# Kernel optimization log

Measured on AMD Instinct MI355X. Metric: run time of the kernel, lower is better.

Reference implementation:

```python
import jax, jax.numpy as jnp
import numpy as np

B, N, H, DQK, DV = 2, 2048, 16, 128, 128
E = H * DV
CHUNK = 64


def setup_inputs() -> dict:
    key = jax.random.key(0)
    ks = jax.random.split(key, 11)
    w = lambda k: jax.random.normal(k, (E, E), jnp.float32) * 0.02
    return {
        "x": jax.random.normal(ks[0], (B, N, E), jnp.float32),
        "prev_state": jnp.zeros((B, H, DQK, DV), jnp.float32),
        "Wq": w(ks[1]), "bq": jnp.zeros((E,), jnp.float32),
        "Wk": w(ks[2]), "bk": jnp.zeros((E,), jnp.float32),
        "Wv": w(ks[3]), "bv": jnp.zeros((E,), jnp.float32),
        "Wg": w(ks[4]), "bg": jnp.zeros((E,), jnp.float32),
        "Wo": w(ks[5]), "bo": jnp.zeros((E,), jnp.float32),
        "start_idx": 0,
    }


def _mul_i(t):
    # multiply interleaved complex pairs by i: (a, b) -> (-b, a)
    t2 = t.reshape(*t.shape[:-1], -1, 2)
    return jnp.stack((-t2[..., 1], t2[..., 0]), axis=-1).reshape(t.shape)


def reference(x, prev_state, Wq, bq, Wk, bk, Wv, bv, Wg, bg, Wo, bo, start_idx):
    b, n, e = x.shape
    h, dqk, dv, c = H, DQK, DV, CHUNK
    q = (x @ Wq.T + bq).reshape(b, n, h, dqk)
    k = (x @ Wk.T + bk).reshape(b, n, h, dqk)
    v = (x @ Wv.T + bv).reshape(b, n, h, dv)

    # xPos-style theta shift (rotary on interleaved pairs), applied along the sequence dim
    lin = jnp.linspace(0.0, 1.0, dqk // 2)
    thetas = jnp.repeat(1.0 / (10000.0 ** lin), 2).astype(x.dtype)  # (dqk,)
    idx = (start_idx + jnp.arange(n)).astype(x.dtype)
    ang = idx[:, None] * thetas[None, :]  # (n, dqk)
    sin = jnp.sin(ang)[None, :, None, :]
    cos = jnp.cos(ang)[None, :, None, :]
    q = q * cos + _mul_i(q) * sin
    k = k * cos + _mul_i(k) * sin
    k = k / jnp.sqrt(jnp.asarray(dqk, x.dtype))

    # per-head decays: 1 - 2^(-5 - h)
    gamma = 1.0 - jnp.exp2(-5.0 - jnp.arange(h, dtype=x.dtype))  # (h,)
    i = jnp.arange(c, dtype=x.dtype)
    mask = i[:, None] >= i[None, :]
    Dmat = jnp.where(mask, gamma[:, None, None] ** jnp.where(mask, i[:, None] - i[None, :], 0.0), 0.0)  # (h,c,c)
    cross_decay = gamma[:, None] ** (i[None, :] + 1.0)   # (h,c)
    kv_decay = gamma[:, None] ** (c - 1.0 - i[None, :])  # (h,c)
    chunk_decay = gamma ** c                              # (h,)

    nc = n // c
    qc = q.reshape(b, nc, c, h, dqk).transpose(1, 0, 3, 2, 4)  # (nc,b,h,c,dqk)
    kc = k.reshape(b, nc, c, h, dqk).transpose(1, 0, 3, 2, 4)
    vc = v.reshape(b, nc, c, h, dv).transpose(1, 0, 3, 2, 4)

    def step(S, qkv):
        qi, ki, vi = qkv  # (b,h,c,d)
        att = jnp.einsum('bhid,bhjd->bhij', qi, ki) * Dmat[None]
        o = jnp.einsum('bhij,bhje->bhie', att, vi)
        o = o + jnp.einsum('bhid,bhde->bhie', qi, S) * cross_decay[None, :, :, None]
        S_new = S * chunk_decay[None, :, None, None] + jnp.einsum('bhjd,bhje->bhde', ki * kv_decay[None, :, :, None], vi)
        return S_new, o

    state, outs = jax.lax.scan(step, prev_state, (qc, kc, vc))
    ret = outs.transpose(1, 0, 3, 2, 4).reshape(b, n, h, dv)

    # GroupNorm(num_groups=h, affine=False): normalize each head over dv
    mu = ret.mean(-1, keepdims=True)
    var = ((ret - mu) ** 2).mean(-1, keepdims=True)
    ret = ((ret - mu) / jnp.sqrt(var + 1e-6)).reshape(b, n, e)

    gate = jax.nn.silu(x @ Wg.T + bg)
    out = (ret * gate) @ Wo.T + bo
    return out, state
```

## Files before the change

kernel.cpp:

```cpp
#include <hip/hip_runtime.h>
#include <hip/hip_bf16.h>
#include <stdint.h>

#define B_   2
#define N_   2048
#define H_   16
#define DQK_ 128
#define DV_  128
#define E_   2048
#define CH_  64
#define NC_  32
#define M_   (B_*N_)
#define QKVG_LD 8192
#define ROT_C 0.21091607f
#define KS_   0.08838834764831843f

using bf16x8 = __attribute__((ext_vector_type(8))) __bf16;
using f32x4  = __attribute__((ext_vector_type(4))) float;
typedef __hip_bfloat16 bf16_t;

__device__ __forceinline__ void gload_lds16(const void* g, void* l) {
  __builtin_amdgcn_global_load_lds(
      (const __attribute__((address_space(1))) void*)(uintptr_t)g,
      (__attribute__((address_space(3))) void*)(uint32_t)(uintptr_t)l,
      16, 0, 0);
}

__device__ __forceinline__ float head_log2g(int h) {
  return (float)(log2(1.0 - exp2((double)(-5 - h))));
}

__device__ __forceinline__ float bfu2f(unsigned short u) {
  unsigned int t = (unsigned int)u << 16; float f;
  __builtin_memcpy(&f, &t, 4); return f;
}
__device__ __forceinline__ unsigned short f2bfu(float f) {
  bf16_t b = __float2bfloat16(f);
  unsigned short u; __builtin_memcpy(&u, &b, 2); return u;
}

__global__ __launch_bounds__(256)
void cvt_all_kernel(const float* __restrict__ x,
                    const float* __restrict__ Wq, const float* __restrict__ Wk,
                    const float* __restrict__ Wv, const float* __restrict__ Wg,
                    const float* __restrict__ Wo,
                    const float* __restrict__ bq, const float* __restrict__ bk,
                    const float* __restrict__ bv, const float* __restrict__ bg,
                    const int* __restrict__ startp,
                    bf16_t* __restrict__ xb, bf16_t* __restrict__ wcat,
                    bf16_t* __restrict__ wob, float* __restrict__ bcat,
                    float2* __restrict__ trig) {
  const int NX = 2097152, NW = 1048576;
  int g = blockIdx.x * 256 + threadIdx.x;
  const float* s; bf16_t* d; int si, di;
  if (g < NX) { s = x; si = g; d = xb; di = g; }
  else if (g < NX + 4*NW) {
    int t = g - NX; int r = t / NW; si = t - r*NW;
    s = (r==0) ? Wq : (r==1) ? Wk : (r==2) ? Wv : Wg; d = wcat; di = t;
  } else if (g < NX + 5*NW) {
    si = g - NX - 4*NW; s = Wo; d = wob; di = si;
  } else if (g < NX + 5*NW + 2048) {
    int j = g - (NX + 5*NW);
    int which = j >> 9, i = j & 511;
    const float* bs = (which==0) ? bq : (which==1) ? bk : (which==2) ? bv : bg;
    ((float4*)bcat)[which*512 + i] = ((const float4*)bs)[i];
    return;
  } else {
    int g2 = g - (NX + 5*NW + 2048);
    if (g2 < 131072) {
      int n = g2 >> 6, j = g2 & 63;
      float ang = (float)(startp[0] + n) * exp2f(-ROT_C * (float)j);
      float sn, cn; sincosf(ang, &sn, &cn);
      trig[g2] = make_float2(cn, sn);
    }
    return;
  }
  float4 v = ((const float4*)s)[si];
  ushort4 p;
  p.x = f2bfu(v.x); p.y = f2bfu(v.y); p.z = f2bfu(v.z); p.w = f2bfu(v.w);
  ((ushort4*)d)[di] = p;
}

template<bool OUT_BF16, int NSUB>
__global__ __launch_bounds__(512, 2)
void gemm8_kernel(const bf16_t* __restrict__ A, const bf16_t* __restrict__ Bw,
                  const float* __restrict__ bias, void* __restrict__ Cout,
                  int K, int ldc, int tilesM) {
  extern __shared__ char smem[];
  const int nwg = gridDim.x;
  const int bid = blockIdx.x;
  const int cpx = nwg >> 3;
  const int swz = (bid & 7) * cpx + (bid >> 3);
  const int tm = swz % tilesM, tn = swz / tilesM;
  const int rowT0 = tm * 256, colT0 = tn * (64 * NSUB);
  const int tid = threadIdx.x, wave = tid >> 6, lane = tid & 63;
  const int wr = wave >> 2, wc = wave & 3;
  const int l16 = lane & 15, lhi = lane >> 4;
  const int NKT = K >> 6;

  const int sw = ((tid & 7) * 16) ^ (((tid >> 3) & 7) << 4);
  const size_t aOff = (size_t)(rowT0 + (tid >> 3)) * K + (sw >> 1);
  const size_t bOff = (size_t)(colT0 + (tid >> 3)) * K + (sw >> 1);
  const uint32_t wl = wave * 1024;

  auto stage = [&](int h) {
    const int ktp = h >> 2, r = h & 3, buf = ktp & 1;
    const int k0 = ktp << 6;
    if (r < 2) {
      const uint32_t base = 65536u + buf * (8192u*NSUB) + r * (4096u*NSUB) + wl;
#pragma unroll
      for (int L = 0; L < NSUB/2; L++)
        gload_lds16(Bw + bOff + (size_t)(r * (NSUB*32) + L * 64) * K + k0,
                    smem + base + L * 8192);
    } else {
      const int half = r - 2;
      const uint32_t base = buf * 32768u + half * 16384u + wl;
#pragma unroll
      for (int L = 0; L < 2; L++)
        gload_lds16(A + aOff + (size_t)(half * 128 + L * 64) * K + k0,
                    smem + base + L * 8192);
    }
  };

  for (int h = 0; h < 6; h++) stage(h);
  if constexpr (NSUB == 4) asm volatile("s_waitcnt vmcnt(4)" ::: "memory");
  else                     asm volatile("s_waitcnt vmcnt(2)" ::: "memory");
  __builtin_amdgcn_s_barrier();
  asm volatile("" ::: "memory");
  __builtin_amdgcn_sched_barrier(0);

  f32x4 acc[8][NSUB] = {};
  bf16x8 bfr[NSUB][2], bnx[2][2];

#pragma unroll
  for (int n = 0; n < 2; n++) {
    const int r = wc * (16*NSUB) + n * 16 + l16;
#pragma unroll
    for (int ks = 0; ks < 2; ks++) {
      const int cb = ks * 64 + lhi * 16;
      bnx[n][ks] = *(const bf16x8*)(smem + 65536u + r * 128 + (cb ^ ((r & 7) << 4)));
    }
  }

  for (int kt = 0; kt < NKT; kt++) {
    const int cur = kt & 1;
    const uint32_t aB = cur * 32768u;
    const uint32_t bB = 65536u + cur * (8192u*NSUB);
#pragma unroll
    for (int p = 0; p < 4; p++) {
      if (p == 0) {
#pragma unroll
        for (int n = 0; n < 2; n++)
#pragma unroll
          for (int ks = 0; ks < 2; ks++) bfr[n][ks] = bnx[n][ks];
        if constexpr (NSUB == 4) {
#pragma unroll
          for (int n = 2; n < 4; n++) {
            const int r = wc * (16*NSUB) + n * 16 + l16;
#pragma unroll
            for (int ks = 0; ks < 2; ks++) {
              const int cb = ks * 64 + lhi * 16;
              bfr[n][ks] = *(const bf16x8*)(smem + bB + r * 128 + (cb ^ ((r & 7) << 4)));
            }
          }
        }
      }
      bf16x8 afr[2][2];
#pragma unroll
      for (int mm = 0; mm < 2; mm++) {
        const int r = wr * 128 + p * 32 + mm * 16 + l16;
#pragma unroll
        for (int ks = 0; ks < 2; ks++) {
          const int cb = ks * 64 + lhi * 16;
          afr[mm][ks] = *(const bf16x8*)(smem + aB + r * 128 + (cb ^ ((r & 7) << 4)));
        }
      }
      const int h = 4 * kt + p + 6;
      if (h < 4 * NKT) stage(h);
      __builtin_amdgcn_sched_barrier(0);
      __builtin_amdgcn_s_setprio(1);
#pragma unroll
      for (int mm = 0; mm < 2; mm++)
#pragma unroll
        for (int n = 0; n < NSUB; n++)
#pragma unroll
          for (int ks = 0; ks < 2; ks++)
            acc[2 * p + mm][n] = __builtin_amdgcn_mfma_f32_16x16x32_bf16(
                afr[mm][ks], bfr[n][ks], acc[2 * p + mm][n], 0, 0, 0);
      __builtin_amdgcn_s_setprio(0);
      if (p == 2) {
        if constexpr (NSUB == 4) asm volatile("s_waitcnt vmcnt(6)" ::: "memory");
        else                     asm volatile("s_waitcnt vmcnt(5)" ::: "memory");
      }
      if (p == 3) {
        if (kt < NKT - 2) {
          if constexpr (NSUB == 4) asm volatile("s_waitcnt vmcnt(4)" ::: "memory");
          else                     asm volatile("s_waitcnt vmcnt(2)" ::: "memory");
        } else if (kt == NKT - 2) {
          asm volatile("s_waitcnt vmcnt(0)" ::: "memory");
        }
        if (kt + 1 < NKT) {
          const uint32_t bN = 65536u + ((kt + 1) & 1) * (8192u*NSUB);
#pragma unroll
          for (int n = 0; n < 2; n++) {
            const int r = wc * (16*NSUB) + n * 16 + l16;
#pragma unroll
            for (int ks = 0; ks < 2; ks++) {
              const int cb = ks * 64 + lhi * 16;
              bnx[n][ks] = *(const bf16x8*)(smem + bN + r * 128 + (cb ^ ((r & 7) << 4)));
            }
          }
        }
      }
      __builtin_amdgcn_s_barrier();
      asm volatile("" ::: "memory");
      __builtin_amdgcn_sched_barrier(0);
    }
  }

#pragma unroll
  for (int m = 0; m < 8; m++) {
    const int rbase = rowT0 + wr * 128 + m * 16 + lhi * 4;
#pragma unroll
    for (int n = 0; n < NSUB; n++) {
      const int col = colT0 + wc * (16*NSUB) + n * 16 + l16;
      const float bv = bias[col];
#pragma unroll
      for (int j = 0; j < 4; j++) {
        float v = acc[m][n][j] + bv;
        if (OUT_BF16) ((bf16_t*)Cout)[(size_t)(rbase + j) * ldc + col] = __float2bfloat16(v);
        else          ((float*)Cout)[(size_t)(rbase + j) * ldc + col] = v;
      }
    }
  }
}

__global__ __launch_bounds__(256)
void chunk_kvt_kernel(const bf16_t* __restrict__ kb, const bf16_t* __restrict__ vb,
                      const float2* __restrict__ trig, bf16_t* __restrict__ kvt) {
  __shared__ alignas(16) char lds[32768];
  char* vts = lds;
  char* kts = lds + 16384;

  const int tid = threadIdx.x, wave = tid >> 6, lane = tid & 63;
  const int l16 = lane & 15, lhi = lane >> 4;
  const int blk = blockIdx.x;
  const int bh = blk >> 5, ch = blk & 31;
  const int h = bh & (H_ - 1);
  const float log2g = head_log2g(h);
  const int n0 = ch * 64;

  const size_t bhbase = (size_t)(bh >> 4) * N_ * QKVG_LD + (size_t)h * 128;

#pragma unroll
  for (int it = 0; it < 4; it++) {
    int j = it*16 + (tid >> 4);
    int e0 = (tid & 15) * 8;
    bf16x8 vv = *(const bf16x8*)(vb + bhbase + (size_t)(n0 + j)*QKVG_LD + e0);
    bf16x8 kk = *(const bf16x8*)(kb + bhbase + (size_t)(n0 + j)*QKVG_LD + e0);
    const float2* tr = trig + (size_t)(n0 + j)*64 + (tid & 15)*4;
    float kvd = exp2f((float)(63 - j) * log2g) * KS_;
    float kr[8];
#pragma unroll
    for (int p = 0; p < 4; p++) {
      float2 cs = tr[p];
      float a = (float)kk[2*p], b2 = (float)kk[2*p+1];
      kr[2*p]   = (a*cs.x - b2*cs.y);
      kr[2*p+1] = (b2*cs.x + a*cs.y);
    }
#pragma unroll
    for (int m = 0; m < 8; m++) {
      int e = e0 + m;
      *(__bf16*)(vts + e*128 + ((j*2) ^ ((e&7)<<4))) = vv[m];
      *(__bf16*)(kts + e*128 + ((j*2) ^ ((e&7)<<4))) = (__bf16)(kr[m] * kvd);
    }
  }
  __syncthreads();

  f32x4 acc[2][8] = {};
#pragma unroll
  for (int kk2 = 0; kk2 < 2; kk2++) {
#pragma unroll
    for (int et = 0; et < 2; et++) {
      int e = (2*wave + et)*16 + l16;
      bf16x8 vf = *(const bf16x8*)(vts + e*128 + (((kk2*32 + lhi*8)*2) ^ ((e&7)<<4)));
#pragma unroll
      for (int dt = 0; dt < 8; dt++) {
        int d = dt*16 + l16;
        bf16x8 kf = *(const bf16x8*)(kts + d*128 + (((kk2*32 + lhi*8)*2) ^ ((d&7)<<4)));
        acc[et][dt] = __builtin_amdgcn_mfma_f32_16x16x32_bf16(vf, kf, acc[et][dt], 0, 0, 0);
      }
    }
  }

  const size_t obase = (size_t)blk * 16384;
#pragma unroll
  for (int et = 0; et < 2; et++)
#pragma unroll
    for (int dt = 0; dt < 8; dt++)
#pragma unroll
      for (int j = 0; j < 4; j++) {
        int e = (2*wave + et)*16 + lhi*4 + j;
        int d = dt*16 + l16;
        kvt[obase + e*128 + d] = __float2bfloat16(acc[et][dt][j]);
      }
}

__global__ __launch_bounds__(256)
void state_scan_kernel(const bf16_t* __restrict__ kvt, const float* __restrict__ prev,
                       bf16_t* __restrict__ sbft, float* __restrict__ out_state) {
  int t = blockIdx.x * 256 + threadIdx.x;
  int bh = t >> 13;
  int ed = (t & 8191) * 2;
  int e = ed >> 7, d = ed & 127;
  int h = bh & (H_ - 1);
  const float cdecay = exp2f(64.0f * head_log2g(h));

  float S0 = prev[(size_t)bh*16384 + (size_t)d*128 + e];
  float S1 = prev[(size_t)bh*16384 + (size_t)(d+1)*128 + e];
  size_t boff = ((size_t)bh * (NC_*16384) + ed) >> 1;
  const unsigned int* kv2 = (const unsigned int*)kvt;
  unsigned int* sb2 = (unsigned int*)sbft;
  for (int ch = 0; ch < NC_; ch++) {
    sb2[boff] = (unsigned int)f2bfu(S0) | ((unsigned int)f2bfu(S1) << 16);
    unsigned int kv = kv2[boff];
    S0 = S0 * cdecay + bfu2f((unsigned short)(kv & 0xffff));
    S1 = S1 * cdecay + bfu2f((unsigned short)(kv >> 16));
    boff += 8192;
  }
  out_state[(size_t)bh*16384 + (size_t)d*128 + e]     = S0;
  out_state[(size_t)bh*16384 + (size_t)(d+1)*128 + e] = S1;
}

__global__ __launch_bounds__(256)
void chunk_out_kernel(const bf16_t* __restrict__ qb, const bf16_t* __restrict__ kb,
                      const bf16_t* __restrict__ vb, const bf16_t* __restrict__ gb,
                      const bf16_t* __restrict__ sbft, const float2* __restrict__ trig,
                      bf16_t* __restrict__ gated) {
  __shared__ alignas(16) char lds[24576];
  char* vts = lds;
  char* ats = lds + 16384;

  const int tid = threadIdx.x, wave = tid >> 6, lane = tid & 63;
  const int l16 = lane & 15, lhi = lane >> 4;
  const int blk = blockIdx.x;
  const int bh = blk >> 5, ch = blk & 31;
  const int h = bh & (H_ - 1);
  const int b = bh >> 4;
  const float log2g = head_log2g(h);
  const int n0 = ch * 64;

  const size_t bhbase = (size_t)b * N_ * QKVG_LD + (size_t)h * 128;
  const bf16_t* Srow = sbft + (size_t)blk * 16384;

#pragma unroll
  for (int it = 0; it < 4; it++) {
    int j = it*16 + (tid >> 4);
    int e0 = (tid & 15) * 8;
    bf16x8 vv = *(const bf16x8*)(vb + bhbase + (size_t)(n0 + j)*QKVG_LD + e0);
#pragma unroll
    for (int m = 0; m < 8; m++) {
      int e = e0 + m;
      *(__bf16*)(vts + e*128 + ((j*2) ^ ((e&7)<<4))) = vv[m];
    }
  }

  const float2* trq = trig + (size_t)(n0 + wave*16 + l16)*64;
  bf16x8 qf[4];
#pragma unroll
  for (int dk = 0; dk < 4; dk++) {
    bf16x8 qv = *(const bf16x8*)(qb + bhbase + (size_t)(n0 + wave*16 + l16)*QKVG_LD + dk*32 + lhi*8);
#pragma unroll
    for (int p = 0; p < 4; p++) {
      float2 cs = trq[dk*16 + lhi*4 + p];
      float a = (float)qv[2*p], b2 = (float)qv[2*p+1];
      qf[dk][2*p]   = (__bf16)(a*cs.x - b2*cs.y);
      qf[dk][2*p+1] = (__bf16)(b2*cs.x + a*cs.y);
    }
  }

  f32x4 aacc[4] = {};
#pragma unroll
  for (int jt = 0; jt < 4; jt++) {
    const float2* trk = trig + (size_t)(n0 + jt*16 + l16)*64;
#pragma unroll
    for (int dk = 0; dk < 4; dk++) {
      bf16x8 kv = *(const bf16x8*)(kb + bhbase + (size_t)(n0 + jt*16 + l16)*QKVG_LD + dk*32 + lhi*8);
      bf16x8 kf;
#pragma unroll
      for (int p = 0; p < 4; p++) {
        float2 cs = trk[dk*16 + lhi*4 + p];
        float a = (float)kv[2*p], b2 = (float)kv[2*p+1];
        kf[2*p]   = (__bf16)((a*cs.x - b2*cs.y) * KS_);
        kf[2*p+1] = (__bf16)((b2*cs.x + a*cs.y) * KS_);
      }
      aacc[jt] = __builtin_amdgcn_mfma_f32_16x16x32_bf16(qf[dk], kf, aacc[jt], 0, 0, 0);
    }
  }
#pragma unroll
  for (int jt = 0; jt < 4; jt++)
#pragma unroll
    for (int j = 0; j < 4; j++) {
      int i = wave*16 + lhi*4 + j;
      int jc = jt*16 + l16;
      aacc[jt][j] *= (i >= jc) ? exp2f((float)(i - jc) * log2g) : 0.0f;
    }

#pragma unroll
  for (int jt = 0; jt < 4; jt++)
#pragma unroll
    for (int j = 0; j < 4; j++) {
      int i = wave*16 + lhi*4 + j;
      int jc = jt*16 + l16;
      *(__bf16*)(ats + i*128 + ((jc*2) ^ ((i&7)<<4))) = (__bf16)aacc[jt][j];
    }
  __syncthreads();

  f32x4 oacc[8] = {};
#pragma unroll
  for (int et = 0; et < 8; et++) {
#pragma unroll
    for (int dk = 0; dk < 4; dk++) {
      int e = et*16 + l16;
      bf16x8 sf = *(const bf16x8*)(Srow + e*128 + dk*32 + lhi*8);
      oacc[et] = __builtin_amdgcn_mfma_f32_16x16x32_bf16(qf[dk], sf, oacc[et], 0, 0, 0);
    }
  }
#pragma unroll
  for (int j = 0; j < 4; j++) {
    int i = wave*16 + lhi*4 + j;
    float f = exp2f((float)(i + 1) * log2g);
#pragma unroll
    for (int et = 0; et < 8; et++) oacc[et][j] *= f;
  }

#pragma unroll
  for (int kk2 = 0; kk2 < 2; kk2++) {
    int i = wave*16 + l16;
    bf16x8 af = *(const bf16x8*)(ats + i*128 + (((kk2*32 + lhi*8)*2) ^ ((i&7)<<4)));
#pragma unroll
    for (int et = 0; et < 8; et++) {
      int e = et*16 + l16;
      bf16x8 vf = *(const bf16x8*)(vts + e*128 + (((kk2*32 + lhi*8)*2) ^ ((e&7)<<4)));
      oacc[et] = __builtin_amdgcn_mfma_f32_16x16x32_bf16(af, vf, oacc[et], 0, 0, 0);
    }
  }

#pragma unroll
  for (int j = 0; j < 4; j++) {
    float s = 0.0f, ss = 0.0f;
#pragma unroll
    for (int et = 0; et < 8; et++) {
      float v = oacc[et][j];
      s += v; ss += v * v;
    }
#pragma unroll
    for (int off = 1; off < 16; off <<= 1) {
      s  += __shfl_xor(s, off);
      ss += __shfl_xor(ss, off);
    }
    float mu  = s * (1.0f/128.0f);
    float inv = rsqrtf(ss * (1.0f/128.0f) - mu*mu + 1e-6f);
    const int i = wave*16 + lhi*4 + j;
    const size_t grow = (size_t)b * N_ + (n0 + i);
#pragma unroll
    for (int et = 0; et < 8; et++) {
      const int col = et*16 + l16;
      float g0 = bfu2f(*(const unsigned short*)(gb + grow*QKVG_LD + h*128 + col));
      float r0 = (oacc[et][j] - mu) * inv * (g0 / (1.0f + expf(-g0)));
      *(unsigned short*)(gated + grow*2048 + h*128 + col) = f2bfu(r0);
    }
  }
}

extern "C" void kernel_launch(void* const* d_in, const int* in_sizes, int n_in,
                              void* d_out, int out_size, void* d_ws, size_t ws_size,
                              hipStream_t stream) {
  const float* x    = (const float*)d_in[0];
  const float* prev = (const float*)d_in[1];
  const float* Wq = (const float*)d_in[2];  const float* bq = (const float*)d_in[3];
  const float* Wk = (const float*)d_in[4];  const float* bk = (const float*)d_in[5];
  const float* Wv = (const float*)d_in[6];  const float* bv = (const float*)d_in[7];
  const float* Wg = (const float*)d_in[8];  const float* bg = (const float*)d_in[9];
  const float* Wo = (const float*)d_in[10]; const float* bo = (const float*)d_in[11];
  const int* startp = (const int*)d_in[12];

  float* out = (float*)d_out;
  float* out_state = out + (size_t)B_*N_*E_;
  float2* trig = (float2*)out;

  char* w = (char*)d_ws;
  const size_t XN = (size_t)B_*N_*E_;
  const size_t WN = (size_t)E_*E_;
  bf16_t* xb   = (bf16_t*)w;             w += XN*2;
  bf16_t* qkvg = (bf16_t*)w;             w += (size_t)M_*QKVG_LD*2;
  bf16_t* wob  = (bf16_t*)w;             w += WN*2;
  char*   wcat_region = w;               w += 4*WN*2;
  bf16_t* wcat = (bf16_t*)wcat_region;
  bf16_t* sbft = (bf16_t*)w;             w += (size_t)B_*H_*NC_*16384*2;
  bf16_t* kvt   = (bf16_t*)wcat_region;
  float*  bcat  = (float*)sbft;

  hipFuncSetAttribute(reinterpret_cast<const void*>(gemm8_kernel<true,4>),
                      hipFuncAttributeMaxDynamicSharedMemorySize, 131072);
  hipFuncSetAttribute(reinterpret_cast<const void*>(gemm8_kernel<false,2>),
                      hipFuncAttributeMaxDynamicSharedMemorySize, 98304);

  cvt_all_kernel<<<29192, 256, 0, stream>>>(x, Wq, Wk, Wv, Wg, Wo, bq, bk, bv, bg,
                                            startp, xb, wcat, wob, bcat, trig);

  gemm8_kernel<true,4><<<512, 512, 131072, stream>>>(xb, wcat, bcat, (void*)qkvg,
                                                     E_, QKVG_LD, 16 );

  chunk_kvt_kernel<<<B_*H_*NC_, 256, 0, stream>>>(qkvg + 2048, qkvg + 4096,
                                                  trig, kvt);
  state_scan_kernel<<<1024, 256, 0, stream>>>(kvt, prev, sbft, out_state);
  chunk_out_kernel<<<B_*H_*NC_, 256, 0, stream>>>(qkvg, qkvg + 2048, qkvg + 4096,
                                                  qkvg + 6144, sbft, trig,
                                                  xb );

  gemm8_kernel<false,2><<<256, 512, 98304, stream>>>(xb, wob, bo, (void*)out,
                                                     E_, E_, 16 );
}
```

Measured before the change: 280.5 us.

## Load GEMM B fragments directly from global into registers, drop B LDS staging

Result: slower. 349.1 us (+24.4%).

```diff
diff --git a/kernel.cpp b/kernel.cpp
--- a/kernel.cpp
+++ b/kernel.cpp
@@ -100,71 +100,36 @@
 
   const int sw = ((tid & 7) * 16) ^ (((tid >> 3) & 7) << 4);
   const size_t aOff = (size_t)(rowT0 + (tid >> 3)) * K + (sw >> 1);
-  const size_t bOff = (size_t)(colT0 + (tid >> 3)) * K + (sw >> 1);
   const uint32_t wl = wave * 1024;
-
-  auto stage = [&](int h) {
-    const int ktp = h >> 2, r = h & 3, buf = ktp & 1;
-    const int k0 = ktp << 6;
-    if (r < 2) {
-      const uint32_t base = 65536u + buf * (8192u*NSUB) + r * (4096u*NSUB) + wl;
-#pragma unroll
-      for (int L = 0; L < NSUB/2; L++)
-        gload_lds16(Bw + bOff + (size_t)(r * (NSUB*32) + L * 64) * K + k0,
-                    smem + base + L * 8192);
-    } else {
-      const int half = r - 2;
-      const uint32_t base = buf * 32768u + half * 16384u + wl;
-#pragma unroll
-      for (int L = 0; L < 2; L++)
-        gload_lds16(A + aOff + (size_t)(half * 128 + L * 64) * K + k0,
-                    smem + base + L * 8192);
-    }
+  const bf16_t* bGlob = Bw + (size_t)(colT0 + wc * (16*NSUB) + l16) * K + lhi * 8;
+
+  auto stageA = [&](int ktp, int half) {
+    const uint32_t base = (uint32_t)(ktp & 1) * 32768u + half * 16384u + wl;
+#pragma unroll
+    for (int L = 0; L < 2; L++)
+      gload_lds16(A + aOff + (size_t)(half * 128 + L * 64) * K + (ktp << 6),
+                  smem + base + L * 8192);
   };
 
-  for (int h = 0; h < 6; h++) stage(h);
-  if constexpr (NSUB == 4) asm volatile("s_waitcnt vmcnt(4)" ::: "memory");
-  else                     asm volatile("s_waitcnt vmcnt(2)" ::: "memory");
+  f32x4 acc[8][NSUB] = {};
+  bf16x8 bA[NSUB][2], bB[NSUB][2];
+
+  stageA(0, 0); stageA(0, 1);
+  __builtin_amdgcn_sched_barrier(0);
+#pragma unroll
+  for (int n = 0; n < NSUB; n++)
+#pragma unroll
+    for (int ks = 0; ks < 2; ks++)
+      bA[n][ks] = *(const bf16x8*)(bGlob + (size_t)(n * 16) * K + ks * 32);
+  asm volatile("s_waitcnt vmcnt(0)" ::: "memory");
   __builtin_amdgcn_s_barrier();
   asm volatile("" ::: "memory");
   __builtin_amdgcn_sched_barrier(0);
 
-  f32x4 acc[8][NSUB] = {};
-  bf16x8 bfr[NSUB][2], bnx[2][2];
-
-#pragma unroll
-  for (int n = 0; n < 2; n++) {
-    const int r = wc * (16*NSUB) + n * 16 + l16;
-#pragma unroll
-    for (int ks = 0; ks < 2; ks++) {
-      const int cb = ks * 64 + lhi * 16;
-      bnx[n][ks] = *(const bf16x8*)(smem + 65536u + r * 128 + (cb ^ ((r & 7) << 4)));
-    }
-  }
-
-  for (int kt = 0; kt < NKT; kt++) {
-    const int cur = kt & 1;
-    const uint32_t aB = cur * 32768u;
-    const uint32_t bB = 65536u + cur * (8192u*NSUB);
+  auto tile = [&](int kt, bf16x8 (&bc)[NSUB][2], bf16x8 (&bn)[NSUB][2]) {
+    const uint32_t aBase = (uint32_t)(kt & 1) * 32768u;
 #pragma unroll
     for (int p = 0; p < 4; p++) {
-      if (p == 0) {
-#pragma unroll
-        for (int n = 0; n < 2; n++)
-#pragma unroll
-          for (int ks = 0; ks < 2; ks++) bfr[n][ks] = bnx[n][ks];
-        if constexpr (NSUB == 4) {
-#pragma unroll
-          for (int n = 2; n < 4; n++) {
-            const int r = wc * (16*NSUB) + n * 16 + l16;
-#pragma unroll
-            for (int ks = 0; ks < 2; ks++) {
-              const int cb = ks * 64 + lhi * 16;
-              bfr[n][ks] = *(const bf16x8*)(smem + bB + r * 128 + (cb ^ ((r & 7) << 4)));
-            }
-          }
-        }
-      }
       bf16x8 afr[2][2];
 #pragma unroll
       for (int mm = 0; mm < 2; mm++) {
@@ -172,11 +137,21 @@
 #pragma unroll
         for (int ks = 0; ks < 2; ks++) {
           const int cb = ks * 64 + lhi * 16;
-          afr[mm][ks] = *(const bf16x8*)(smem + aB + r * 128 + (cb ^ ((r & 7) << 4)));
+          afr[mm][ks] = *(const bf16x8*)(smem + aBase + r * 128 + (cb ^ ((r & 7) << 4)));
         }
       }
-      const int h = 4 * kt + p + 6;
-      if (h < 4 * NKT) stage(h);
+      if (p < 2) {
+        if (kt + 1 < NKT) stageA(kt + 1, p);
+      } else if (p == 2) {
+        if (kt + 1 < NKT) {
+          const bf16_t* bsrc = bGlob + (size_t)(kt + 1) * 64;
+#pragma unroll
+          for (int n = 0; n < NSUB; n++)
+#pragma unroll
+            for (int ks = 0; ks < 2; ks++)
+              bn[n][ks] = *(const bf16x8*)(bsrc + (size_t)(n * 16) * K + ks * 32);
+        }
+      }
       __builtin_amdgcn_sched_barrier(0);
       __builtin_amdgcn_s_setprio(1);
 #pragma unroll
@@ -186,36 +161,23 @@
 #pragma unroll
           for (int ks = 0; ks < 2; ks++)
             acc[2 * p + mm][n] = __builtin_amdgcn_mfma_f32_16x16x32_bf16(
-                afr[mm][ks], bfr[n][ks], acc[2 * p + mm][n], 0, 0, 0);
+                afr[mm][ks], bc[n][ks], acc[2 * p + mm][n], 0, 0, 0);
       __builtin_amdgcn_s_setprio(0);
-      if (p == 2) {
-        if constexpr (NSUB == 4) asm volatile("s_waitcnt vmcnt(6)" ::: "memory");
-        else                     asm volatile("s_waitcnt vmcnt(5)" ::: "memory");
-      }
       if (p == 3) {
-        if (kt < NKT - 2) {
-          if constexpr (NSUB == 4) asm volatile("s_waitcnt vmcnt(4)" ::: "memory");
-          else                     asm volatile("s_waitcnt vmcnt(2)" ::: "memory");
-        } else if (kt == NKT - 2) {
-          asm volatile("s_waitcnt vmcnt(0)" ::: "memory");
+        if (kt + 1 < NKT) {
+          if constexpr (NSUB == 4) asm volatile("s_waitcnt vmcnt(8)" ::: "memory");
+          else                     asm volatile("s_waitcnt vmcnt(4)" ::: "memory");
         }
-        if (kt + 1 < NKT) {
-          const uint32_t bN = 65536u + ((kt + 1) & 1) * (8192u*NSUB);
-#pragma unroll
-          for (int n = 0; n < 2; n++) {
-            const int r = wc * (16*NSUB) + n * 16 + l16;
-#pragma unroll
-            for (int ks = 0; ks < 2; ks++) {
-              const int cb = ks * 64 + lhi * 16;
-              bnx[n][ks] = *(const bf16x8*)(smem + bN + r * 128 + (cb ^ ((r & 7) << 4)));
-            }
-          }
-        }
-      }
-      __builtin_amdgcn_s_barrier();
-      asm volatile("" ::: "memory");
-      __builtin_amdgcn_sched_barrier(0);
-    }
+        __builtin_amdgcn_s_barrier();
+        asm volatile("" ::: "memory");
+        __builtin_amdgcn_sched_barrier(0);
+      }
+    }
+  };
+
+  for (int kt = 0; kt < NKT; kt += 2) {
+    tile(kt,     bA, bB);
+    tile(kt + 1, bB, bA);
   }
 
 #pragma unroll
@@ -502,15 +464,15 @@
   float*  bcat  = (float*)sbft;
 
   hipFuncSetAttribute(reinterpret_cast<const void*>(gemm8_kernel<true,4>),
-                      hipFuncAttributeMaxDynamicSharedMemorySize, 131072);
+                      hipFuncAttributeMaxDynamicSharedMemorySize, 65536);
   hipFuncSetAttribute(reinterpret_cast<const void*>(gemm8_kernel<false,2>),
-                      hipFuncAttributeMaxDynamicSharedMemorySize, 98304);
+                      hipFuncAttributeMaxDynamicSharedMemorySize, 65536);
 
   cvt_all_kernel<<<29192, 256, 0, stream>>>(x, Wq, Wk, Wv, Wg, Wo, bq, bk, bv, bg,
                                             startp, xb, wcat, wob, bcat, trig);
 
-  gemm8_kernel<true,4><<<512, 512, 131072, stream>>>(xb, wcat, bcat, (void*)qkvg,
-                                                     E_, QKVG_LD, 16 );
+  gemm8_kernel<true,4><<<512, 512, 65536, stream>>>(xb, wcat, bcat, (void*)qkvg,
+                                                    E_, QKVG_LD, 16 );
 
   chunk_kvt_kernel<<<B_*H_*NC_, 256, 0, stream>>>(qkvg + 2048, qkvg + 4096,
                                                   trig, kvt);
@@ -519,6 +481,6 @@
                                                   qkvg + 6144, sbft, trig,
                                                   xb );
 
-  gemm8_kernel<false,2><<<256, 512, 98304, stream>>>(xb, wob, bo, (void*)out,
+  gemm8_kernel<false,2><<<256, 512, 65536, stream>>>(xb, wob, bo, (void*)out,
                                                      E_, E_, 16 );
 }
```
